# Kernel tuning notes

Measured on AMD Instinct MI355X. Metric: run time of the kernel, lower is better.

## Reference

```python
import jax, jax.numpy as jnp
import numpy as np

N = 50000       # nodes
E = 800000      # edges (before self-loops)
NFEAT = 256
NHID = 16       # per-head hidden dim
HEADS = 8
NCLASS = 16
NEG_SLOPE = 0.2  # PyG GATConv default leaky-relu slope


def setup_inputs() -> dict:
    key = jax.random.key(0)
    ks = jax.random.split(key, 10)
    s = 0.05  # weight scale for numerical sanity
    return {
        "x": jax.random.normal(ks[0], (N, NFEAT), jnp.float32),
        "edge_index": jax.random.randint(ks[1], (2, E), 0, N, dtype=jnp.int32),
        "W1": jax.random.normal(ks[2], (NFEAT, HEADS * NHID), jnp.float32) * s,
        "att_src1": jax.random.normal(ks[3], (HEADS, NHID), jnp.float32) * s,
        "att_dst1": jax.random.normal(ks[4], (HEADS, NHID), jnp.float32) * s,
        "b1": jnp.zeros((HEADS * NHID,), jnp.float32),
        "W2": jax.random.normal(ks[5], (HEADS * NHID, NCLASS), jnp.float32) * s,
        "att_src2": jax.random.normal(ks[6], (1, NCLASS), jnp.float32) * s,
        "att_dst2": jax.random.normal(ks[7], (1, NCLASS), jnp.float32) * s,
        "b2": jnp.zeros((NCLASS,), jnp.float32),
    }


def gat_conv(x, edge_index, W, a_src, a_dst, b, heads, out_c, concat):
    """Faithful PyG GATConv (eval mode: dropout off, add_self_loops=True)."""
    n = x.shape[0]
    loop = jnp.arange(n, dtype=edge_index.dtype)
    src = jnp.concatenate([edge_index[0], loop])  # [E+N]
    dst = jnp.concatenate([edge_index[1], loop])  # [E+N]
    h = (x @ W).reshape(n, heads, out_c)          # [N, H, C]
    # per-node attention logits
    alpha_src = jnp.einsum('nhc,hc->nh', h, a_src)  # [N, H]
    alpha_dst = jnp.einsum('nhc,hc->nh', h, a_dst)  # [N, H]
    e = jax.nn.leaky_relu(alpha_src[src] + alpha_dst[dst], NEG_SLOPE)  # [E+N, H]
    # segment softmax over incoming edges of each dst node (self-loop guarantees nonempty)
    m = jax.lax.stop_gradient(jax.ops.segment_max(e, dst, num_segments=n))
    p = jnp.exp(e - m[dst])
    denom = jax.ops.segment_sum(p, dst, num_segments=n)
    a = p / denom[dst]                              # [E+N, H]
    out = jax.ops.segment_sum(a[:, :, None] * h[src], dst, num_segments=n)  # [N, H, C]
    out = out.reshape(n, heads * out_c) if concat else out.mean(axis=1)
    return out + b


def reference(x, edge_index, W1, att_src1, att_dst1, b1, W2, att_src2, att_dst2, b2):
    h1 = jax.nn.elu(gat_conv(x, edge_index, W1, att_src1, att_dst1, b1, HEADS, NHID, True))
    return gat_conv(h1, edge_index, W2, att_src2, att_dst2, b2, 1, NCLASS, False)
```

## Files before the change

### kernel.cpp

```cpp
#include <hip/hip_runtime.h>
#include <hip/hip_bf16.h>

#define NNODES 50000
#define NEDGES 800000
#define NFEATS 256
#define NHID 16
#define HEADS 8
#define NCLS 16
#define NEG_SLOPE 0.2f
#define TOTE (NEDGES + NNODES)
#define RSTRIDE 64
#define NBUCK 196
#define NPB 256
#define BCAP 4864
#define S1_EPT 16
#define BIN_BLOCKS ((TOTE + 4095) / 4096)
#define GSTRIDE 16
#define GEMM1_BLOCKS ((NNODES + 127) / 128)

typedef __attribute__((ext_vector_type(8))) short short8;
typedef __attribute__((ext_vector_type(4))) float floatx4;

static __device__ __forceinline__ short f2bf(float f) {
    __hip_bfloat16 b = __float2bfloat16(f);
    return *reinterpret_cast<short*>(&b);
}

#define AS1 __attribute__((address_space(1)))
#define AS3 __attribute__((address_space(3)))

static __device__ __forceinline__ void ld_lds16(const void* g, void* l) {
#if __has_builtin(__builtin_amdgcn_global_load_lds)
    __builtin_amdgcn_global_load_lds((const AS1 void*)g, (AS3 void*)l, 16, 0, 0);
#endif
}


__global__ __launch_bounds__(256) void k_bin(const int* __restrict__ ei,
                                             int* __restrict__ gcnt, int* __restrict__ barr,
                                             const float* __restrict__ W,
                                             const float* __restrict__ a_s,
                                             const float* __restrict__ a_d,
                                             short* __restrict__ Wsw) {
    int tid = threadIdx.x;
    if (blockIdx.x >= BIN_BLOCKS) {
        int t = (blockIdx.x - BIN_BLOCKS) * 256 + tid;
        if (t >= 4608) return;
        short8 b;
        if (t < 4096) {
            int kc = t >> 9, nt = (t >> 6) & 7, lane = t & 63;
            int quad = lane >> 4, lo = lane & 15;
#pragma unroll
            for (int j = 0; j < 8; j++)
                b[j] = f2bf(W[(size_t)(kc * 32 + quad * 8 + j) * 128 + nt * 16 + lo]);
        } else {
            int t2 = t - 4096;
            int kc = t2 >> 6, lane = t2 & 63;
            int quad = lane >> 4, lo = lane & 15;
            int h = lo & 7;
            const float* av = (lo < 8) ? (a_s + h * 16) : (a_d + h * 16);
#pragma unroll
            for (int j = 0; j < 8; j++) {
                int k = kc * 32 + quad * 8 + j;
                float acc = 0.f;
#pragma unroll
                for (int c = 0; c < 16; c++) acc += W[(size_t)k * 128 + h * 16 + c] * av[c];
                b[j] = f2bf(acc);
            }
        }
        *(short8*)(Wsw + (size_t)t * 8) = b;
        return;
    }

    __shared__ int lcnt[NBUCK], lbase[NBUCK];
    if (tid < NBUCK) lcnt[tid] = 0;
    __syncthreads();
    int e0 = blockIdx.x * (256 * S1_EPT) + tid;
    int s[S1_EPT], d[S1_EPT], rk[S1_EPT];
#pragma unroll
    for (int k = 0; k < S1_EPT; k++) {
        int e = e0 + k * 256;
        bool v = e < TOTE;
        int ss = 0, dd = 0;
        if (v) {
            if (e < NEDGES) { ss = ei[e]; dd = ei[NEDGES + e]; }
            else            { ss = e - NEDGES; dd = ss; }
        }
        s[k] = ss; d[k] = dd;
        rk[k] = v ? atomicAdd(&lcnt[dd >> 8], 1) : -1;
    }
    __syncthreads();
    if (tid < NBUCK) lbase[tid] = lcnt[tid] ? atomicAdd(&gcnt[tid * GSTRIDE], lcnt[tid]) : 0;
    __syncthreads();
#pragma unroll
    for (int k = 0; k < S1_EPT; k++) {
        if (rk[k] >= 0) {
            int b = d[k] >> 8;
            int pos = lbase[b] + rk[k];
            if (pos < BCAP)
                barr[(size_t)b * BCAP + pos] = ((d[k] & 255) << 16) | s[k];
        }
    }
}


__global__ __launch_bounds__(256) void k_mid(const int* __restrict__ gcnt,
                                             const int* __restrict__ barr,
                                             int* __restrict__ cnt, unsigned short* __restrict__ csr,
                                             const float* __restrict__ x,
                                             const short* __restrict__ Wsw,
                                             __hip_bfloat16* __restrict__ h1,
                                             float* __restrict__ as1, float* __restrict__ ad1) {
    __shared__ short smem[32768];
    int tid = threadIdx.x;

    if (blockIdx.x < NBUCK) {
        int* lcnt = (int*)smem;
        unsigned short* lcsr = (unsigned short*)smem + 512;
        int b = blockIdx.x;
        lcnt[tid] = 0;
        __syncthreads();
        int n = min(gcnt[b * GSTRIDE], BCAP);
        int nodeBase = b << 8;
        for (int i = tid; i < n; i += 256) {
            int e = barr[(size_t)b * BCAP + i];
            int ln = e >> 16;
            int r = atomicAdd(&lcnt[ln], 1);
            if (r < RSTRIDE) lcsr[ln * 65 + r] = (unsigned short)(e & 0xFFFF);
        }
        __syncthreads();
        int node = nodeBase + tid;
        if (node < NNODES) cnt[node] = min(lcnt[tid], RSTRIDE);
        for (int i = tid; i < NPB * RSTRIDE; i += 256) {
            int ln = i >> 6;
            int nn = nodeBase + ln;
            if (nn < NNODES && (i & 63) < min(lcnt[ln], RSTRIDE))
                csr[(size_t)nodeBase * RSTRIDE + i] = lcsr[ln * 65 + (i & 63)];
        }
        return;
    }

    short* bsw = smem;
    int bid  = blockIdx.x - NBUCK;
    int wave = tid >> 6;
    int lane = tid & 63;
    int quad = lane >> 4;
    int lo   = lane & 15;

#if __has_builtin(__builtin_amdgcn_global_load_lds)
    {
        const char* gsrc = (const char*)Wsw + (size_t)wave * 1024 + (size_t)lane * 16;
        char* ldst = (char*)bsw + wave * 1024;
#pragma unroll
        for (int it = 0; it < 16; it++)
            ld_lds16(gsrc + it * 4096, ldst + it * 4096);
    }
#else
    {
        const uint4* g4 = (const uint4*)Wsw;
        uint4* l4 = (uint4*)bsw;
#pragma unroll
        for (int it = 0; it < 16; it++) l4[it * 256 + tid] = g4[it * 256 + tid];
    }
#endif
    short8 wafr[8];
#pragma unroll
    for (int kc = 0; kc < 8; kc++)
        wafr[kc] = *(const short8*)(Wsw + (size_t)(4096 + kc * 64 + lane) * 8);
    __syncthreads();

    int rowBase = bid * 128 + wave * 32;
    const float* xa[2];
#pragma unroll
    for (int mt = 0; mt < 2; mt++) {
        int row = rowBase + mt * 16 + lo;
        row = (row < NNODES) ? row : (NNODES - 1);
        xa[mt] = x + (size_t)row * 256 + quad * 8;
    }

    floatx4 acc[2][8], accA[2];
#pragma unroll
    for (int mt = 0; mt < 2; mt++) {
        accA[mt] = (floatx4){0.f, 0.f, 0.f, 0.f};
#pragma unroll
        for (int nt = 0; nt < 8; nt++) acc[mt][nt] = (floatx4){0.f, 0.f, 0.f, 0.f};
    }

    float4 a0[2], a1[2];
#pragma unroll
    for (int mt = 0; mt < 2; mt++) {
        a0[mt] = *(const float4*)(xa[mt]);
        a1[mt] = *(const float4*)(xa[mt] + 4);
    }

    for (int kc = 0; kc < 8; kc++) {
        float4 n0[2], n1[2];
        if (kc < 7) {
#pragma unroll
            for (int mt = 0; mt < 2; mt++) {
                n0[mt] = *(const float4*)(xa[mt] + (kc + 1) * 32);
                n1[mt] = *(const float4*)(xa[mt] + (kc + 1) * 32 + 4);
            }
        }
        short8 afr[2];
#pragma unroll
        for (int mt = 0; mt < 2; mt++) {
            union { short8 s; __hip_bfloat162 h[4]; } u;
            u.h[0] = __float22bfloat162_rn(make_float2(a0[mt].x, a0[mt].y));
            u.h[1] = __float22bfloat162_rn(make_float2(a0[mt].z, a0[mt].w));
            u.h[2] = __float22bfloat162_rn(make_float2(a1[mt].x, a1[mt].y));
            u.h[3] = __float22bfloat162_rn(make_float2(a1[mt].z, a1[mt].w));
            afr[mt] = u.s;
        }
#pragma unroll
        for (int nt = 0; nt < 8; nt++) {
            short8 bfr = *(const short8*)&bsw[((kc * 8 + nt) * 64 + lane) * 8];
            acc[0][nt] = __builtin_amdgcn_mfma_f32_16x16x32_bf16(afr[0], bfr, acc[0][nt], 0, 0, 0);
            acc[1][nt] = __builtin_amdgcn_mfma_f32_16x16x32_bf16(afr[1], bfr, acc[1][nt], 0, 0, 0);
        }
        accA[0] = __builtin_amdgcn_mfma_f32_16x16x32_bf16(afr[0], wafr[kc], accA[0], 0, 0, 0);
        accA[1] = __builtin_amdgcn_mfma_f32_16x16x32_bf16(afr[1], wafr[kc], accA[1], 0, 0, 0);
#pragma unroll
        for (int mt = 0; mt < 2; mt++) { a0[mt] = n0[mt]; a1[mt] = n1[mt]; }
    }

#pragma unroll
    for (int mt = 0; mt < 2; mt++)
#pragma unroll
        for (int nt = 0; nt < 8; nt++)
#pragma unroll
            for (int reg = 0; reg < 4; reg++) {
                int row = rowBase + mt * 16 + quad * 4 + reg;
                int col = nt * 16 + lo;
                if (row < NNODES)
                    h1[(size_t)row * 128 + col] = __float2bfloat16(acc[mt][nt][reg]);
            }
#pragma unroll
    for (int mt = 0; mt < 2; mt++)
#pragma unroll
        for (int reg = 0; reg < 4; reg++) {
            int row = rowBase + mt * 16 + quad * 4 + reg;
            if (row < NNODES) {
                float v = accA[mt][reg];
                if (lo < 8) as1[(size_t)row * 8 + lo] = v;
                else        ad1[(size_t)row * 8 + (lo - 8)] = v;
            }
        }
}


__global__ __launch_bounds__(256) void k_aggA(const int* __restrict__ cnt,
                                              const unsigned short* __restrict__ csr,
                                              const __hip_bfloat16* __restrict__ h1,
                                              const float* __restrict__ as1, const float* __restrict__ ad1,
                                              const float* __restrict__ b1,
                                              const float* __restrict__ W2,
                                              const float* __restrict__ a_s2,
                                              const float* __restrict__ a_d2,
                                              float* __restrict__ h2,
                                              float* __restrict__ as2, float* __restrict__ ad2) {
    __shared__ float w2t[16 * 132];
    __shared__ float vbuf[4 * 4 * 132];
    int tid = threadIdx.x;
#pragma unroll
    for (int i = 0; i < 8; i++) {
        int e = i * 256 + tid;
        w2t[(e & 15) * 132 + (e >> 4)] = W2[e];
    }
    __syncthreads();

    int wavid = tid >> 6;
    int lane  = tid & 63;
    int cl    = lane & 15;
    int nd    = lane >> 4;
    int node  = (blockIdx.x * 4 + wavid) * 4 + nd;
    int head  = cl >> 1;
    int deg   = min(cnt[node], RSTRIDE);
    float adst = ad1[node * 8 + head];
    int rs = node * RSTRIDE;
    int rowv[4];
#pragma unroll
    for (int r = 0; r < 4; r++) rowv[r] = csr[rs + cl + 16 * r];
    int md = deg;
    md = max(md, __shfl_xor(md, 16));
    md = max(md, __shfl_xor(md, 32));

    float acc[8] = {0.f, 0.f, 0.f, 0.f, 0.f, 0.f, 0.f, 0.f};
    float s = 0.f;
#pragma unroll
    for (int r = 0; r < 4; r++) {
        int rbase = r << 4;
        if (rbase >= md) break;
        int lim = min(16, md - rbase);
        for (int i2 = 0; i2 < lim; i2 += 4) {
            float p[4];
            union { short8 v; __hip_bfloat162 h[4]; } u[4];
#pragma unroll
            for (int t = 0; t < 4; t++) {
                int idx = rbase + i2 + t;
                int src = __shfl(rowv[r], (lane & 48) | ((i2 + t) & 15));
                p[t] = 0.f;
                u[t].v = (short8){0, 0, 0, 0, 0, 0, 0, 0};
                if (idx < deg) {
                    u[t].v = *(const short8*)(h1 + (size_t)src * 128 + cl * 8);
                    float e = as1[src * 8 + head] + adst;
                    e = (e > 0.f) ? e : NEG_SLOPE * e;
                    p[t] = __expf(e);
                }
            }
            s += (p[0] + p[1]) + (p[2] + p[3]);
#pragma unroll
            for (int t = 0; t < 4; t++)
#pragma unroll
                for (int q = 0; q < 4; q++) {
                    float2 f = __bfloat1622float2(u[t].h[q]);
                    acc[q * 2]     = fmaf(p[t], f.x, acc[q * 2]);
                    acc[q * 2 + 1] = fmaf(p[t], f.y, acc[q * 2 + 1]);
                }
        }
    }
    float is = 1.f / s;
    float v[8];
#pragma unroll
    for (int q = 0; q < 8; q++) {
        float t = acc[q] * is + b1[cl * 8 + q];
        v[q] = (t > 0.f) ? t : (__expf(t) - 1.f);
    }
    float* vb = &vbuf[(wavid * 4 + nd) * 132 + cl * 8];
    *(float4*)vb       = make_float4(v[0], v[1], v[2], v[3]);
    *(float4*)(vb + 4) = make_float4(v[4], v[5], v[6], v[7]);

    const float* vrow = &vbuf[(wavid * 4 + nd) * 132];
    const float* wrow = &w2t[cl * 132];
    float outp = 0.f;
#pragma unroll
    for (int j = 0; j < 128; j += 4) {
        float4 vv = *(const float4*)(vrow + j);
        float4 ww = *(const float4*)(wrow + j);
        outp = fmaf(vv.x, ww.x, outp);
        outp = fmaf(vv.y, ww.y, outp);
        outp = fmaf(vv.z, ww.z, outp);
        outp = fmaf(vv.w, ww.w, outp);
    }
    h2[(size_t)node * 16 + cl] = outp;

    float sv = outp * a_s2[cl];
    float dv = outp * a_d2[cl];
#pragma unroll
    for (int o = 1; o <= 8; o <<= 1) {
        sv += __shfl_xor(sv, o);
        dv += __shfl_xor(dv, o);
    }
    if (cl == 0) { as2[node] = sv; ad2[node] = dv; }
}


__global__ __launch_bounds__(256) void k_agg2(const int* __restrict__ cnt,
                                              const unsigned short* __restrict__ csr,
                                              const float* __restrict__ h2, const float* __restrict__ as2,
                                              const float* __restrict__ ad2, const float* __restrict__ b2,
                                              float* __restrict__ out) {
    int tid   = threadIdx.x;
    int wavid = tid >> 6;
    int lane  = tid & 63;
    int nd    = lane >> 4;
    int sub   = lane & 15;
    int slot  = sub >> 2;
    int c4    = sub & 3;
    int node  = (blockIdx.x * 4 + wavid) * 4 + nd;
    int deg   = min(cnt[node], RSTRIDE);
    float adst = ad2[node];
    int rs = node * RSTRIDE;
    int rowv[4];
#pragma unroll
    for (int r = 0; r < 4; r++) rowv[r] = csr[rs + sub + 16 * r];
    int md = deg;
    md = max(md, __shfl_xor(md, 16));
    md = max(md, __shfl_xor(md, 32));

    float4 acc = make_float4(0.f, 0.f, 0.f, 0.f);
    float s = 0.f;
#pragma unroll
    for (int r = 0; r < 4; r++) {
        int rbase = r << 4;
        if (rbase >= md) break;
        int lim = min(16, md - rbase);
        for (int i2 = 0; i2 < lim; i2 += 8) {
            int ia = rbase + i2 + slot;
            int ib = ia + 4;
            int sa = __shfl(rowv[r], (lane & 48) | (i2 + slot));
            int sb = __shfl(rowv[r], (lane & 48) | (i2 + 4 + slot));
            float p0 = 0.f, p1 = 0.f;
            float4 r0 = make_float4(0.f, 0.f, 0.f, 0.f);
            float4 r1 = make_float4(0.f, 0.f, 0.f, 0.f);
            if (ia < deg) {
                r0 = *(const float4*)(h2 + (size_t)sa * 16 + c4 * 4);
                float e = as2[sa] + adst;
                e = (e > 0.f) ? e : NEG_SLOPE * e;
                p0 = __expf(e);
            }
            if (ib < deg) {
                r1 = *(const float4*)(h2 + (size_t)sb * 16 + c4 * 4);
                float e = as2[sb] + adst;
                e = (e > 0.f) ? e : NEG_SLOPE * e;
                p1 = __expf(e);
            }
            s += p0 + p1;
            acc.x = fmaf(p0, r0.x, fmaf(p1, r1.x, acc.x));
            acc.y = fmaf(p0, r0.y, fmaf(p1, r1.y, acc.y));
            acc.z = fmaf(p0, r0.z, fmaf(p1, r1.z, acc.z));
            acc.w = fmaf(p0, r0.w, fmaf(p1, r1.w, acc.w));
        }
    }
#pragma unroll
    for (int o = 4; o <= 8; o <<= 1) {
        acc.x += __shfl_xor(acc.x, o);
        acc.y += __shfl_xor(acc.y, o);
        acc.z += __shfl_xor(acc.z, o);
        acc.w += __shfl_xor(acc.w, o);
        s += __shfl_xor(s, o);
    }
    if (slot == 0) {
        float is = 1.f / s;
        float4 o4;
        o4.x = acc.x * is + b2[c4 * 4 + 0];
        o4.y = acc.y * is + b2[c4 * 4 + 1];
        o4.z = acc.z * is + b2[c4 * 4 + 2];
        o4.w = acc.w * is + b2[c4 * 4 + 3];
        *(float4*)(out + (size_t)node * 16 + c4 * 4) = o4;
    }
}


extern "C" void kernel_launch(void* const* d_in, const int* in_sizes, int n_in,
                              void* d_out, int out_size, void* d_ws, size_t ws_size,
                              hipStream_t stream) {
    const float* x    = (const float*)d_in[0];
    const int*   ei   = (const int*)d_in[1];
    const float* W1   = (const float*)d_in[2];
    const float* a_s1 = (const float*)d_in[3];
    const float* a_d1 = (const float*)d_in[4];
    const float* b1   = (const float*)d_in[5];
    const float* W2   = (const float*)d_in[6];
    const float* a_s2 = (const float*)d_in[7];
    const float* a_d2 = (const float*)d_in[8];
    const float* b2   = (const float*)d_in[9];
    float* out = (float*)d_out;

    char* p = (char*)d_ws;
    auto alloc = [&](size_t bytes) -> char* {
        char* q = p;
        p += (bytes + 255) & ~(size_t)255;
        return q;
    };
    int*  gcnt = (int*)alloc((size_t)NBUCK * GSTRIDE * 4);
    int*  barr = (int*)alloc((size_t)NBUCK * BCAP * 4);
    int*  cnt  = (int*)alloc((size_t)NNODES * 4);
    unsigned short* csr = (unsigned short*)alloc((size_t)NNODES * RSTRIDE * 2);
    short* Wsw = (short*)alloc((size_t)36864 * 2);
    __hip_bfloat16* h1 = (__hip_bfloat16*)alloc((size_t)NNODES * 128 * 2);
    float* as1 = (float*)alloc((size_t)NNODES * 8 * 4);
    float* ad1 = (float*)alloc((size_t)NNODES * 8 * 4);
    float* h2  = (float*)alloc((size_t)NNODES * 16 * 4);
    float* as2 = (float*)barr;
    float* ad2 = (float*)barr + NNODES;

    hipMemsetAsync(gcnt, 0, (size_t)NBUCK * GSTRIDE * 4, stream);
    hipLaunchKernelGGL(k_bin,  dim3(BIN_BLOCKS + 18), dim3(256), 0, stream,
                       ei, gcnt, barr, W1, a_s1, a_d1, Wsw);
    hipLaunchKernelGGL(k_mid,  dim3(NBUCK + GEMM1_BLOCKS), dim3(256), 0, stream,
                       gcnt, barr, cnt, csr, x, Wsw, h1, as1, ad1);
    hipLaunchKernelGGL(k_aggA, dim3(NNODES / 16), dim3(256), 0, stream,
                       cnt, csr, h1, as1, ad1, b1, W2, a_s2, a_d2, h2, as2, ad2);
    hipLaunchKernelGGL(k_agg2, dim3(NNODES / 16), dim3(256), 0, stream, cnt, csr, h2, as2, ad2, b2, out);
}
```

Measured before the change: 187.5 us.

## Replace two-pass bucketed CSR build with direct global-atomic scatter

The two-stage bucket sort (block-local binning, then a per-bucket LDS CSR assembly fused with the GEMM kernel) is replaced by a single scatter kernel. In that kernel each edge does a global atomicAdd on its destination's count and writes its source straight into a fixed-stride CSR row. This drops the intermediate bucket array and one pass over the edges. In exchange it relies on 850k global atomics on random addresses, which contend and cost latency, and the GEMM no longer overlaps with the CSR assembly. The order of neighbours within a row is now nondeterministic.

```diff
diff --git a/kernel.cpp b/kernel.cpp
--- a/kernel.cpp
+++ b/kernel.cpp
@@ -10,12 +10,7 @@
 #define NEG_SLOPE 0.2f
 #define TOTE (NEDGES + NNODES)
 #define RSTRIDE 64
-#define NBUCK 196
-#define NPB 256
-#define BCAP 4864
-#define S1_EPT 16
-#define BIN_BLOCKS ((TOTE + 4095) / 4096)
-#define GSTRIDE 16
+#define SCAT_BLOCKS 831
 #define GEMM1_BLOCKS ((NNODES + 127) / 128)
 
 typedef __attribute__((ext_vector_type(8))) short short8;
@@ -36,15 +31,16 @@
 }
 
 
-__global__ __launch_bounds__(256) void k_bin(const int* __restrict__ ei,
-                                             int* __restrict__ gcnt, int* __restrict__ barr,
-                                             const float* __restrict__ W,
-                                             const float* __restrict__ a_s,
-                                             const float* __restrict__ a_d,
-                                             short* __restrict__ Wsw) {
+__global__ __launch_bounds__(256) void k_scat(const int* __restrict__ ei,
+                                              int* __restrict__ cnt,
+                                              unsigned short* __restrict__ csr,
+                                              const float* __restrict__ W,
+                                              const float* __restrict__ a_s,
+                                              const float* __restrict__ a_d,
+                                              short* __restrict__ Wsw) {
     int tid = threadIdx.x;
-    if (blockIdx.x >= BIN_BLOCKS) {
-        int t = (blockIdx.x - BIN_BLOCKS) * 256 + tid;
+    if (blockIdx.x >= SCAT_BLOCKS) {
+        int t = (blockIdx.x - SCAT_BLOCKS) * 256 + tid;
         if (t >= 4608) return;
         short8 b;
         if (t < 4096) {
@@ -72,76 +68,27 @@
         return;
     }
 
-    __shared__ int lcnt[NBUCK], lbase[NBUCK];
-    if (tid < NBUCK) lcnt[tid] = 0;
-    __syncthreads();
-    int e0 = blockIdx.x * (256 * S1_EPT) + tid;
-    int s[S1_EPT], d[S1_EPT], rk[S1_EPT];
-#pragma unroll
-    for (int k = 0; k < S1_EPT; k++) {
+    int e0 = blockIdx.x * 1024 + tid;
+#pragma unroll
+    for (int k = 0; k < 4; k++) {
         int e = e0 + k * 256;
-        bool v = e < TOTE;
-        int ss = 0, dd = 0;
-        if (v) {
+        if (e < TOTE) {
+            int ss, dd;
             if (e < NEDGES) { ss = ei[e]; dd = ei[NEDGES + e]; }
             else            { ss = e - NEDGES; dd = ss; }
-        }
-        s[k] = ss; d[k] = dd;
-        rk[k] = v ? atomicAdd(&lcnt[dd >> 8], 1) : -1;
-    }
-    __syncthreads();
-    if (tid < NBUCK) lbase[tid] = lcnt[tid] ? atomicAdd(&gcnt[tid * GSTRIDE], lcnt[tid]) : 0;
-    __syncthreads();
-#pragma unroll
-    for (int k = 0; k < S1_EPT; k++) {
-        if (rk[k] >= 0) {
-            int b = d[k] >> 8;
-            int pos = lbase[b] + rk[k];
-            if (pos < BCAP)
-                barr[(size_t)b * BCAP + pos] = ((d[k] & 255) << 16) | s[k];
-        }
-    }
-}
-
-
-__global__ __launch_bounds__(256) void k_mid(const int* __restrict__ gcnt,
-                                             const int* __restrict__ barr,
-                                             int* __restrict__ cnt, unsigned short* __restrict__ csr,
-                                             const float* __restrict__ x,
-                                             const short* __restrict__ Wsw,
-                                             __hip_bfloat16* __restrict__ h1,
-                                             float* __restrict__ as1, float* __restrict__ ad1) {
-    __shared__ short smem[32768];
-    int tid = threadIdx.x;
-
-    if (blockIdx.x < NBUCK) {
-        int* lcnt = (int*)smem;
-        unsigned short* lcsr = (unsigned short*)smem + 512;
-        int b = blockIdx.x;
-        lcnt[tid] = 0;
-        __syncthreads();
-        int n = min(gcnt[b * GSTRIDE], BCAP);
-        int nodeBase = b << 8;
-        for (int i = tid; i < n; i += 256) {
-            int e = barr[(size_t)b * BCAP + i];
-            int ln = e >> 16;
-            int r = atomicAdd(&lcnt[ln], 1);
-            if (r < RSTRIDE) lcsr[ln * 65 + r] = (unsigned short)(e & 0xFFFF);
-        }
-        __syncthreads();
-        int node = nodeBase + tid;
-        if (node < NNODES) cnt[node] = min(lcnt[tid], RSTRIDE);
-        for (int i = tid; i < NPB * RSTRIDE; i += 256) {
-            int ln = i >> 6;
-            int nn = nodeBase + ln;
-            if (nn < NNODES && (i & 63) < min(lcnt[ln], RSTRIDE))
-                csr[(size_t)nodeBase * RSTRIDE + i] = lcsr[ln * 65 + (i & 63)];
-        }
-        return;
-    }
-
-    short* bsw = smem;
-    int bid  = blockIdx.x - NBUCK;
+            int r = atomicAdd(&cnt[dd], 1);
+            if (r < RSTRIDE) csr[(size_t)dd * RSTRIDE + r] = (unsigned short)ss;
+        }
+    }
+}
+
+
+__global__ __launch_bounds__(256) void k_gemm1(const float* __restrict__ x,
+                                               const short* __restrict__ Wsw,
+                                               __hip_bfloat16* __restrict__ h1,
+                                               float* __restrict__ as1, float* __restrict__ ad1) {
+    __shared__ short bsw[32768];
+    int tid  = threadIdx.x;
     int wave = tid >> 6;
     int lane = tid & 63;
     int quad = lane >> 4;
@@ -169,7 +116,7 @@
         wafr[kc] = *(const short8*)(Wsw + (size_t)(4096 + kc * 64 + lane) * 8);
     __syncthreads();
 
-    int rowBase = bid * 128 + wave * 32;
+    int rowBase = blockIdx.x * 128 + wave * 32;
     const float* xa[2];
 #pragma unroll
     for (int mt = 0; mt < 2; mt++) {
@@ -453,8 +400,6 @@
         p += (bytes + 255) & ~(size_t)255;
         return q;
     };
-    int*  gcnt = (int*)alloc((size_t)NBUCK * GSTRIDE * 4);
-    int*  barr = (int*)alloc((size_t)NBUCK * BCAP * 4);
     int*  cnt  = (int*)alloc((size_t)NNODES * 4);
     unsigned short* csr = (unsigned short*)alloc((size_t)NNODES * RSTRIDE * 2);
     short* Wsw = (short*)alloc((size_t)36864 * 2);
@@ -462,15 +407,16 @@
     float* as1 = (float*)alloc((size_t)NNODES * 8 * 4);
     float* ad1 = (float*)alloc((size_t)NNODES * 8 * 4);
     float* h2  = (float*)alloc((size_t)NNODES * 16 * 4);
-    float* as2 = (float*)barr;
-    float* ad2 = (float*)barr + NNODES;
-
-    hipMemsetAsync(gcnt, 0, (size_t)NBUCK * GSTRIDE * 4, stream);
-    hipLaunchKernelGGL(k_bin,  dim3(BIN_BLOCKS + 18), dim3(256), 0, stream,
-                       ei, gcnt, barr, W1, a_s1, a_d1, Wsw);
-    hipLaunchKernelGGL(k_mid,  dim3(NBUCK + GEMM1_BLOCKS), dim3(256), 0, stream,
-                       gcnt, barr, cnt, csr, x, Wsw, h1, as1, ad1);
-    hipLaunchKernelGGL(k_aggA, dim3(NNODES / 16), dim3(256), 0, stream,
+    float* as2 = (float*)alloc((size_t)NNODES * 4);
+    float* ad2 = (float*)alloc((size_t)NNODES * 4);
+
+    hipMemsetAsync(cnt, 0, (size_t)NNODES * 4, stream);
+    hipLaunchKernelGGL(k_scat,  dim3(SCAT_BLOCKS + 18), dim3(256), 0, stream,
+                       ei, cnt, csr, W1, a_s1, a_d1, Wsw);
+    hipLaunchKernelGGL(k_gemm1, dim3(GEMM1_BLOCKS), dim3(256), 0, stream,
+                       x, Wsw, h1, as1, ad1);
+    hipLaunchKernelGGL(k_aggA,  dim3(NNODES / 16), dim3(256), 0, stream,
                        cnt, csr, h1, as1, ad1, b1, W2, a_s2, a_d2, h2, as2, ad2);
-    hipLaunchKernelGGL(k_agg2, dim3(NNODES / 16), dim3(256), 0, stream, cnt, csr, h2, as2, ad2, b2, out);
-}
+    hipLaunchKernelGGL(k_agg2,  dim3(NNODES / 16), dim3(256), 0, stream,
+                       cnt, csr, h2, as2, ad2, b2, out);
+}
```

Measured after the change: 225.2 us. 1.2x slower.

## Split GEMM1 column halves across block pairs and shrink binning work per thread

Applied to the files above, without the earlier changes.

The first-layer GEMM blocks now each compute half of the 128 output columns, so twice as many blocks are launched. Each block stages only its half of the weight tile plus the attention-projection weights in a smaller LDS buffer, and only the even half computes the attention logits. Binning now handles 4 edges per thread instead of 16, which launches more bin blocks, and k_mid gains an occupancy hint of 4 blocks per CU. The aim is more parallelism and occupancy for the memory-bound GEMM, at the cost of each x row being read twice and the two halves doing unequal work.

```diff
diff --git a/kernel.cpp b/kernel.cpp
--- a/kernel.cpp
+++ b/kernel.cpp
@@ -13,10 +13,10 @@
 #define NBUCK 196
 #define NPB 256
 #define BCAP 4864
-#define S1_EPT 16
-#define BIN_BLOCKS ((TOTE + 4095) / 4096)
+#define S1_EPT 4
+#define BIN_BLOCKS ((TOTE + 1023) / 1024)
 #define GSTRIDE 16
-#define GEMM1_BLOCKS ((NNODES + 127) / 128)
+#define GEMM1_BLOCKS 782
 
 typedef __attribute__((ext_vector_type(8))) short short8;
 typedef __attribute__((ext_vector_type(4))) float floatx4;
@@ -104,14 +104,14 @@
 }
 
 
-__global__ __launch_bounds__(256) void k_mid(const int* __restrict__ gcnt,
+__global__ __launch_bounds__(256, 4) void k_mid(const int* __restrict__ gcnt,
                                              const int* __restrict__ barr,
                                              int* __restrict__ cnt, unsigned short* __restrict__ csr,
                                              const float* __restrict__ x,
                                              const short* __restrict__ Wsw,
                                              __hip_bfloat16* __restrict__ h1,
                                              float* __restrict__ as1, float* __restrict__ ad1) {
-    __shared__ short smem[32768];
+    __shared__ short smem[20480];
     int tid = threadIdx.x;
 
     if (blockIdx.x < NBUCK) {
@@ -140,8 +140,9 @@
         return;
     }
 
-    short* bsw = smem;
+    short8* bsw8 = (short8*)smem;
     int bid  = blockIdx.x - NBUCK;
+    int h    = bid & 1;
     int wave = tid >> 6;
     int lane = tid & 63;
     int quad = lane >> 4;
@@ -149,27 +150,45 @@
 
 #if __has_builtin(__builtin_amdgcn_global_load_lds)
     {
-        const char* gsrc = (const char*)Wsw + (size_t)wave * 1024 + (size_t)lane * 16;
-        char* ldst = (char*)bsw + wave * 1024;
-#pragma unroll
-        for (int it = 0; it < 16; it++)
-            ld_lds16(gsrc + it * 4096, ldst + it * 4096);
+        const char* wb = (const char*)Wsw;
+        char* lb = (char*)smem;
+#pragma unroll
+        for (int it = 0; it < 8; it++) {
+            int c = it * 4 + wave;
+            int kc = c >> 2, ntl = c & 3;
+            ld_lds16(wb + ((size_t)((kc * 8 + h * 4 + ntl) * 64) * 16) + lane * 16,
+                     lb + c * 1024);
+        }
+        if (h == 0) {
+#pragma unroll
+            for (int it = 0; it < 2; it++) {
+                int wc = it * 4 + wave;
+                ld_lds16(wb + ((size_t)((4096 + wc * 64)) * 16) + lane * 16,
+                         lb + (2048 + wc * 64) * 16);
+            }
+        }
     }
 #else
     {
-        const uint4* g4 = (const uint4*)Wsw;
-        uint4* l4 = (uint4*)bsw;
-#pragma unroll
-        for (int it = 0; it < 16; it++) l4[it * 256 + tid] = g4[it * 256 + tid];
+        const short8* g8 = (const short8*)Wsw;
+#pragma unroll
+        for (int it = 0; it < 8; it++) {
+            int c = it * 4 + wave;
+            int kc = c >> 2, ntl = c & 3;
+            bsw8[c * 64 + lane] = g8[(kc * 8 + h * 4 + ntl) * 64 + lane];
+        }
+        if (h == 0) {
+#pragma unroll
+            for (int it = 0; it < 2; it++) {
+                int wc = it * 4 + wave;
+                bsw8[2048 + wc * 64 + lane] = g8[4096 + wc * 64 + lane];
+            }
+        }
     }
 #endif
-    short8 wafr[8];
-#pragma unroll
-    for (int kc = 0; kc < 8; kc++)
-        wafr[kc] = *(const short8*)(Wsw + (size_t)(4096 + kc * 64 + lane) * 8);
     __syncthreads();
 
-    int rowBase = bid * 128 + wave * 32;
+    int rowBase = (bid >> 1) * 128 + wave * 32;
     const float* xa[2];
 #pragma unroll
     for (int mt = 0; mt < 2; mt++) {
@@ -178,12 +197,12 @@
         xa[mt] = x + (size_t)row * 256 + quad * 8;
     }
 
-    floatx4 acc[2][8], accA[2];
+    floatx4 acc[2][4], accA[2];
 #pragma unroll
     for (int mt = 0; mt < 2; mt++) {
         accA[mt] = (floatx4){0.f, 0.f, 0.f, 0.f};
 #pragma unroll
-        for (int nt = 0; nt < 8; nt++) acc[mt][nt] = (floatx4){0.f, 0.f, 0.f, 0.f};
+        for (int nt = 0; nt < 4; nt++) acc[mt][nt] = (floatx4){0.f, 0.f, 0.f, 0.f};
     }
 
     float4 a0[2], a1[2];
@@ -213,13 +232,16 @@
             afr[mt] = u.s;
         }
 #pragma unroll
-        for (int nt = 0; nt < 8; nt++) {
-            short8 bfr = *(const short8*)&bsw[((kc * 8 + nt) * 64 + lane) * 8];
+        for (int nt = 0; nt < 4; nt++) {
+            short8 bfr = bsw8[(kc * 4 + nt) * 64 + lane];
             acc[0][nt] = __builtin_amdgcn_mfma_f32_16x16x32_bf16(afr[0], bfr, acc[0][nt], 0, 0, 0);
             acc[1][nt] = __builtin_amdgcn_mfma_f32_16x16x32_bf16(afr[1], bfr, acc[1][nt], 0, 0, 0);
         }
-        accA[0] = __builtin_amdgcn_mfma_f32_16x16x32_bf16(afr[0], wafr[kc], accA[0], 0, 0, 0);
-        accA[1] = __builtin_amdgcn_mfma_f32_16x16x32_bf16(afr[1], wafr[kc], accA[1], 0, 0, 0);
+        if (h == 0) {
+            short8 wbfr = bsw8[2048 + kc * 64 + lane];
+            accA[0] = __builtin_amdgcn_mfma_f32_16x16x32_bf16(afr[0], wbfr, accA[0], 0, 0, 0);
+            accA[1] = __builtin_amdgcn_mfma_f32_16x16x32_bf16(afr[1], wbfr, accA[1], 0, 0, 0);
+        }
 #pragma unroll
         for (int mt = 0; mt < 2; mt++) { a0[mt] = n0[mt]; a1[mt] = n1[mt]; }
     }
@@ -227,25 +249,27 @@
 #pragma unroll
     for (int mt = 0; mt < 2; mt++)
 #pragma unroll
-        for (int nt = 0; nt < 8; nt++)
+        for (int nt = 0; nt < 4; nt++)
 #pragma unroll
             for (int reg = 0; reg < 4; reg++) {
                 int row = rowBase + mt * 16 + quad * 4 + reg;
-                int col = nt * 16 + lo;
+                int col = h * 64 + nt * 16 + lo;
                 if (row < NNODES)
                     h1[(size_t)row * 128 + col] = __float2bfloat16(acc[mt][nt][reg]);
             }
-#pragma unroll
-    for (int mt = 0; mt < 2; mt++)
-#pragma unroll
-        for (int reg = 0; reg < 4; reg++) {
-            int row = rowBase + mt * 16 + quad * 4 + reg;
-            if (row < NNODES) {
-                float v = accA[mt][reg];
-                if (lo < 8) as1[(size_t)row * 8 + lo] = v;
-                else        ad1[(size_t)row * 8 + (lo - 8)] = v;
-            }
-        }
+    if (h == 0) {
+#pragma unroll
+        for (int mt = 0; mt < 2; mt++)
+#pragma unroll
+            for (int reg = 0; reg < 4; reg++) {
+                int row = rowBase + mt * 16 + quad * 4 + reg;
+                if (row < NNODES) {
+                    float v = accA[mt][reg];
+                    if (lo < 8) as1[(size_t)row * 8 + lo] = v;
+                    else        ad1[(size_t)row * 8 + (lo - 8)] = v;
+                }
+            }
+    }
 }
 
 
```

New measurement: 199.7 us. 6.5% more time.
